# Optimization experiments

Measured on AMD Instinct MI355X. Metric: run time of the kernel, lower is better.

## Reference

```python
import jax, jax.numpy as jnp
import numpy as np

NUM_USERS = 100000
NUM_MOVIES = 50000
NUM_NODES = NUM_USERS + NUM_MOVIES
EMB_DIM = 64
N_LAYERS = 3
N_EDGES = 4000000


def setup_inputs() -> dict:
    key = jax.random.key(0)
    k_e, k_w = jax.random.split(key)
    edge_index = jax.random.randint(k_e, (2, N_EDGES), 0, NUM_NODES, dtype=jnp.int64 if jax.config.jax_enable_x64 else jnp.int32)
    emb_weight = jax.random.normal(k_w, (NUM_NODES, EMB_DIM), dtype=jnp.float32)
    return {"edge_index": edge_index, "emb_weight": emb_weight}


def reference(edge_index, emb_weight):
    row, col = edge_index[0], edge_index[1]
    num_nodes = emb_weight.shape[0]
    # degree of each node as a scatter-add destination (col)
    deg = jax.ops.segment_sum(jnp.ones_like(col, dtype=emb_weight.dtype), col,
                              num_segments=num_nodes)
    deg_inv_sqrt = jnp.where(deg > 0, jax.lax.rsqrt(jnp.maximum(deg, 1.0)), 0.0)
    deg_inv_sqrt = jnp.where(deg > 0, deg ** -0.5, 0.0)
    norm = deg_inv_sqrt[row] * deg_inv_sqrt[col]  # [E]

    embs = emb_weight
    acc = emb_weight  # running sum for the final mean over layers
    for _ in range(N_LAYERS):
        msgs = norm[:, None] * embs[row]  # [E, D] gather + scale
        embs = jax.ops.segment_sum(msgs, col, num_segments=num_nodes)  # [N, D]
        acc = acc + embs
    return acc / (N_LAYERS + 1)
```

## Files before the change

kernel.cpp:

```cpp
#include <hip/hip_runtime.h>
#include <hip/hip_fp16.h>

#define D 64
constexpr int TPB = 256;
constexpr int PTPB = 512;
constexpr int CTPB = 1024;
constexpr int VSHIFT = 8;
constexpr int VNODES = 1 << VSHIFT;
constexpr int CHUNK = 8192;
constexpr int CAP = 8192;
constexpr int MAXBUK = 640;
constexpr int GPAD = 16;
typedef unsigned short u16;

__device__ inline unsigned h2pack(float a, float b) {
    unsigned lo = __half_as_ushort(__float2half_rn(a));
    unsigned hi = __half_as_ushort(__float2half_rn(b));
    return lo | (hi << 16);
}

__global__ void fuseAB_kernel(const int* __restrict__ row, const int* __restrict__ col,
                              int* __restrict__ gcnt, unsigned* __restrict__ tmp,
                              int E, int NBUK) {
    __shared__ int h[MAXBUK];
    __shared__ int cur[MAXBUK];
    int t = threadIdx.x, blk = blockIdx.x;
    for (int b = t; b < NBUK; b += PTPB) h[b] = 0;
    __syncthreads();
    int base = blk * CHUNK;
    int n = min(CHUNK, E - base);
    for (int i = t; i < n; i += PTPB)
        atomicAdd(&h[col[base + i] >> VSHIFT], 1);
    __syncthreads();
    for (int b = t; b < NBUK; b += PTPB) {
        int c = h[b];
        cur[b] = (c > 0) ? atomicAdd(&gcnt[b * GPAD], c) : 0;
    }
    __syncthreads();
    for (int i = t; i < n; i += PTPB) {
        int c = col[base + i];
        int b = c >> VSHIFT;
        int p = atomicAdd(&cur[b], 1);
        if (p < CAP)
            tmp[(size_t)b * CAP + p] =
                ((unsigned)(c & (VNODES - 1)) << 18) | (unsigned)row[base + i];
    }
}

__global__ void bscan_kernel(const int* __restrict__ gcnt, int* __restrict__ bExcl, int nb) {
    __shared__ int s[1024];
    int t = threadIdx.x;
    int v = (t < nb) ? gcnt[t * GPAD] : 0;
    s[t] = v;
    __syncthreads();
    for (int off = 1; off < 1024; off <<= 1) {
        int x = (t >= off) ? s[t - off] : 0;
        __syncthreads();
        s[t] += x;
        __syncthreads();
    }
    if (t < nb) bExcl[t] = s[t] - v;
}

__global__ void passC_kernel(const unsigned* __restrict__ tmp, const int* __restrict__ gcnt,
                             const int* __restrict__ bExcl,
                             int* __restrict__ row_ptr, float* __restrict__ dis,
                             int* __restrict__ srow,
                             const float2* __restrict__ emb2, unsigned* __restrict__ A,
                             int N, int E) {
    __shared__ int cnt[VNODES], sc[VNODES], cur[VNODES];
    int b = blockIdx.x, t = threadIdx.x;
    int nodeBase = b << VSHIFT;
    if (t < VNODES) cnt[t] = 0;
    if (b == 0 && t < 32) A[(size_t)N * 32 + t] = 0;
    __syncthreads();
    int m = min(gcnt[b * GPAD], CAP);
    const unsigned* __restrict__ tb = tmp + (size_t)b * CAP;
    for (int i = t; i < m; i += CTPB)
        atomicAdd(&cnt[tb[i] >> 18], 1);
    __syncthreads();
    if (t < VNODES) sc[t] = cnt[t];
    __syncthreads();
    for (int off = 1; off < VNODES; off <<= 1) {
        int i = (t + 1) * (off << 1) - 1;
        if (i < VNODES) sc[i] += sc[i - off];
        __syncthreads();
    }
    if (t == 0) sc[VNODES - 1] = 0;
    __syncthreads();
    for (int off = VNODES / 2; off >= 1; off >>= 1) {
        int i = (t + 1) * (off << 1) - 1;
        if (i < VNODES) { int x = sc[i - off]; sc[i - off] = sc[i]; sc[i] += x; }
        __syncthreads();
    }
    int gbase = bExcl[b];
    if (t < VNODES) {
        int rp = gbase + sc[t];
        cur[t] = rp;
        int node = nodeBase + t;
        if (node < N) {
            row_ptr[node] = rp;
            int d = cnt[t];
            dis[node] = (d > 0) ? rsqrtf((float)d) : 0.0f;
        }
    }
    if (b == 0 && t == 0) row_ptr[N] = E;
    __syncthreads();
    for (int i = t; i < m; i += CTPB) {
        unsigned pk = tb[i];
        int p = atomicAdd(&cur[pk >> 18], 1);
        srow[p] = (int)(pk & 0x3FFFFu);
    }
    for (int i = t; i < (VNODES << 5); i += CTPB) {
        int k = i >> 5;
        int node = nodeBase + k;
        if (node < N) {
            int d = cnt[k];
            float dv = (d > 0) ? rsqrtf((float)d) : 0.0f;
            size_t o = (size_t)node * 32 + (i & 31);
            float2 x = emb2[o];
            A[o] = h2pack(dv * x.x, dv * x.y);
        }
    }
}

#define ACC8(u) do { \
    a0 += __half2float(__ushort_as_half((u16)((u).x & 0xffff))); \
    a1 += __half2float(__ushort_as_half((u16)((u).x >> 16)));    \
    a2 += __half2float(__ushort_as_half((u16)((u).y & 0xffff))); \
    a3 += __half2float(__ushort_as_half((u16)((u).y >> 16)));    \
    a4 += __half2float(__ushort_as_half((u16)((u).z & 0xffff))); \
    a5 += __half2float(__ushort_as_half((u16)((u).z >> 16)));    \
    a6 += __half2float(__ushort_as_half((u16)((u).w & 0xffff))); \
    a7 += __half2float(__ushort_as_half((u16)((u).w >> 16)));    \
} while (0)

template <int MODE, bool WRITE_DST>
__global__ void spmm_kernel(const int* __restrict__ row_ptr, const int* __restrict__ srow,
                            const float* __restrict__ dis,
                            const unsigned* __restrict__ src, unsigned* __restrict__ dst,
                            float2* __restrict__ out2, const float2* __restrict__ emb2,
                            int N) {
    if (WRITE_DST && blockIdx.x == 0 && threadIdx.x < 32)
        dst[(size_t)N * 32 + threadIdx.x] = 0;
    int wave = (blockIdx.x * blockDim.x + threadIdx.x) >> 6;
    int lane = threadIdx.x & 63;
    int half = lane >> 5;
    int sub  = lane & 31;
    int node = 2 * wave + half;
    if (node >= N) return;
    int start = row_ptr[node];
    int end   = row_ptr[node + 1];
    int hb = half << 5;
    int rg = sub >> 3;
    int q  = sub & 7;
    const uint4* __restrict__ s4 = (const uint4*)src;
    float a0 = 0, a1 = 0, a2 = 0, a3 = 0, a4 = 0, a5 = 0, a6 = 0, a7 = 0;
    for (int base = start; base < end; base += 32) {
        int mye = base + sub;
        int rr = (mye < end) ? srow[mye] : 0;
        int cnt = end - base;
        int r0 = __shfl(rr, hb +  0 + rg);
        int r1 = __shfl(rr, hb +  4 + rg);
        int r2 = __shfl(rr, hb +  8 + rg);
        int r3 = __shfl(rr, hb + 12 + rg);
        int r4 = __shfl(rr, hb + 16 + rg);
        int r5 = __shfl(rr, hb + 20 + rg);
        int r6 = __shfl(rr, hb + 24 + rg);
        int r7 = __shfl(rr, hb + 28 + rg);
        r0 = ( 0 + rg < cnt) ? r0 : N;
        r1 = ( 4 + rg < cnt) ? r1 : N;
        r2 = ( 8 + rg < cnt) ? r2 : N;
        r3 = (12 + rg < cnt) ? r3 : N;
        r4 = (16 + rg < cnt) ? r4 : N;
        r5 = (20 + rg < cnt) ? r5 : N;
        r6 = (24 + rg < cnt) ? r6 : N;
        r7 = (28 + rg < cnt) ? r7 : N;
        uint4 u0 = s4[(size_t)r0 * 8 + q];
        uint4 u1 = s4[(size_t)r1 * 8 + q];
        uint4 u2 = s4[(size_t)r2 * 8 + q];
        uint4 u3 = s4[(size_t)r3 * 8 + q];
        uint4 u4 = s4[(size_t)r4 * 8 + q];
        uint4 u5 = s4[(size_t)r5 * 8 + q];
        uint4 u6 = s4[(size_t)r6 * 8 + q];
        uint4 u7 = s4[(size_t)r7 * 8 + q];
        ACC8(u0); ACC8(u1); ACC8(u2); ACC8(u3);
        ACC8(u4); ACC8(u5); ACC8(u6); ACC8(u7);
    }
    a0 += __shfl_xor(a0, 8);  a1 += __shfl_xor(a1, 8);
    a2 += __shfl_xor(a2, 8);  a3 += __shfl_xor(a3, 8);
    a4 += __shfl_xor(a4, 8);  a5 += __shfl_xor(a5, 8);
    a6 += __shfl_xor(a6, 8);  a7 += __shfl_xor(a7, 8);
    a0 += __shfl_xor(a0, 16); a1 += __shfl_xor(a1, 16);
    a2 += __shfl_xor(a2, 16); a3 += __shfl_xor(a3, 16);
    a4 += __shfl_xor(a4, 16); a5 += __shfl_xor(a5, 16);
    a6 += __shfl_xor(a6, 16); a7 += __shfl_xor(a7, 16);
    if (rg != 0) return;
    float dc = dis[node];
    float e0 = dc * a0, e1 = dc * a1, e2 = dc * a2, e3 = dc * a3;
    float e4 = dc * a4, e5 = dc * a5, e6 = dc * a6, e7 = dc * a7;
    if (WRITE_DST) {
        uint4 pk;
        pk.x = h2pack(dc * e0, dc * e1);
        pk.y = h2pack(dc * e2, dc * e3);
        pk.z = h2pack(dc * e4, dc * e5);
        pk.w = h2pack(dc * e6, dc * e7);
        ((uint4*)dst)[(size_t)node * 8 + q] = pk;
    }
    size_t fo = (size_t)node * 16 + q * 2;
    float4* __restrict__ o4 = (float4*)out2;
    float4 c0, c1;
    if (MODE == 0) {
        const float4* __restrict__ e4p = (const float4*)emb2;
        c0 = e4p[fo]; c1 = e4p[fo + 1];
        c0.x += e0; c0.y += e1; c0.z += e2; c0.w += e3;
        c1.x += e4; c1.y += e5; c1.z += e6; c1.w += e7;
    } else if (MODE == 1) {
        c0 = o4[fo]; c1 = o4[fo + 1];
        c0.x += e0; c0.y += e1; c0.z += e2; c0.w += e3;
        c1.x += e4; c1.y += e5; c1.z += e6; c1.w += e7;
    } else {
        c0 = o4[fo]; c1 = o4[fo + 1];
        c0.x = (c0.x + e0) * 0.25f; c0.y = (c0.y + e1) * 0.25f;
        c0.z = (c0.z + e2) * 0.25f; c0.w = (c0.w + e3) * 0.25f;
        c1.x = (c1.x + e4) * 0.25f; c1.y = (c1.y + e5) * 0.25f;
        c1.z = (c1.z + e6) * 0.25f; c1.w = (c1.w + e7) * 0.25f;
    }
    o4[fo] = c0; o4[fo + 1] = c1;
}

extern "C" void kernel_launch(void* const* d_in, const int* in_sizes, int n_in,
                              void* d_out, int out_size, void* d_ws, size_t ws_size,
                              hipStream_t stream) {
    const int* edge = (const int*)d_in[0];
    const float* emb = (const float*)d_in[1];
    const int E = in_sizes[0] / 2;
    const int N = in_sizes[1] / D;
    float2* out2 = (float2*)d_out;

    const int* row = edge;
    const int* col = edge + E;

    const int NBLK = (E + CHUNK - 1) / CHUNK;
    const int NBUK = (N + VNODES - 1) >> VSHIFT;

    size_t zrow = (size_t)(N + 1) * 32;
    size_t tsz  = (size_t)NBUK * CAP;
    size_t bsz  = (tsz > zrow) ? tsz : zrow;
    unsigned* A       = (unsigned*)d_ws;
    unsigned* B       = A + zrow;
    unsigned* tmp     = B;
    int*      srow    = (int*)(B + bsz);
    int*      row_ptr = srow + E;
    float*    dis     = (float*)(row_ptr + N + 1);
    int*      gcnt    = (int*)(dis + N);
    int*      bExcl   = gcnt + NBUK * GPAD;

    const int spmm_blocks = (((N + 1) / 2) * 64 + TPB - 1) / TPB;

    hipMemsetAsync(gcnt, 0, (size_t)NBUK * GPAD * sizeof(int), stream);
    fuseAB_kernel<<<NBLK, PTPB, 0, stream>>>(row, col, gcnt, tmp, E, NBUK);
    bscan_kernel<<<1, 1024, 0, stream>>>(gcnt, bExcl, NBUK);
    passC_kernel<<<NBUK, CTPB, 0, stream>>>(tmp, gcnt, bExcl, row_ptr, dis,
                                            srow, (const float2*)emb, A, N, E);

    spmm_kernel<0, true><<<spmm_blocks, TPB, 0, stream>>>(row_ptr, srow, dis, A, B,
                                                          out2, (const float2*)emb, N);
    spmm_kernel<1, true><<<spmm_blocks, TPB, 0, stream>>>(row_ptr, srow, dis, B, A,
                                                          out2, (const float2*)emb, N);
    spmm_kernel<2, false><<<spmm_blocks, TPB, 0, stream>>>(row_ptr, srow, dis, A, nullptr,
                                                           out2, (const float2*)emb, N);
}
```

Measured before the change: 461.5 us.

## Stage bucketed edges in shared memory for coalesced bucket writes

Measured after the change: 414.5 us. 1.11x faster.

```diff
diff --git a/kernel.cpp b/kernel.cpp
--- a/kernel.cpp
+++ b/kernel.cpp
@@ -3,11 +3,11 @@
 
 #define D 64
 constexpr int TPB = 256;
-constexpr int PTPB = 512;
+constexpr int PTPB = 1024;
 constexpr int CTPB = 1024;
 constexpr int VSHIFT = 8;
 constexpr int VNODES = 1 << VSHIFT;
-constexpr int CHUNK = 8192;
+constexpr int CHUNK = 16384;
 constexpr int CAP = 8192;
 constexpr int MAXBUK = 640;
 constexpr int GPAD = 16;
@@ -22,28 +22,49 @@
 __global__ void fuseAB_kernel(const int* __restrict__ row, const int* __restrict__ col,
                               int* __restrict__ gcnt, unsigned* __restrict__ tmp,
                               int E, int NBUK) {
+    __shared__ unsigned s_stage[CHUNK];
     __shared__ int h[MAXBUK];
-    __shared__ int cur[MAXBUK];
+    __shared__ int s[1024];
+    __shared__ int gbase[MAXBUK];
     int t = threadIdx.x, blk = blockIdx.x;
-    for (int b = t; b < NBUK; b += PTPB) h[b] = 0;
+    for (int b = t; b < MAXBUK; b += PTPB) h[b] = 0;
     __syncthreads();
     int base = blk * CHUNK;
     int n = min(CHUNK, E - base);
     for (int i = t; i < n; i += PTPB)
         atomicAdd(&h[col[base + i] >> VSHIFT], 1);
     __syncthreads();
-    for (int b = t; b < NBUK; b += PTPB) {
-        int c = h[b];
-        cur[b] = (c > 0) ? atomicAdd(&gcnt[b * GPAD], c) : 0;
-    }
+    int v = (t < NBUK) ? h[t] : 0;
+    if (t < NBUK && v > 0) gbase[t] = atomicAdd(&gcnt[t * GPAD], v);
+    s[t] = v;
+    __syncthreads();
+    for (int off = 1; off < 1024; off <<= 1) {
+        int x = (t >= off) ? s[t - off] : 0;
+        __syncthreads();
+        s[t] += x;
+        __syncthreads();
+    }
+    s[t] -= v;
     __syncthreads();
     for (int i = t; i < n; i += PTPB) {
         int c = col[base + i];
         int b = c >> VSHIFT;
-        int p = atomicAdd(&cur[b], 1);
-        if (p < CAP)
-            tmp[(size_t)b * CAP + p] =
-                ((unsigned)(c & (VNODES - 1)) << 18) | (unsigned)row[base + i];
+        int p = atomicAdd(&s[b], 1);
+        s_stage[p] = ((unsigned)(c & (VNODES - 1)) << 18) | (unsigned)row[base + i];
+    }
+    __syncthreads();
+    int w = t >> 6, lane = t & 63;
+    for (int b = w; b < NBUK; b += (PTPB >> 6)) {
+        int cnt = h[b];
+        if (cnt == 0) continue;
+        int lo = s[b] - cnt;
+        int gb = gbase[b];
+        unsigned* __restrict__ dst = tmp + (size_t)b * CAP;
+        for (int j = lane; j < cnt; j += 64) {
+            int p = gb + j;
+            if (p < CAP)
+                dst[p] = s_stage[lo + j];
+        }
     }
 }
 
```
